# Performance work log

Measured on AMD Instinct MI355X. Metric: run time of the kernel, lower is better.

Reference implementation:

```python
import jax, jax.numpy as jnp
import numpy as np

N = 20000   # nodes
E = 320000  # directed edges (before self-loops)
D = 64      # input_dim
H = 10      # GAT heads
HD = H * D  # 640
NEG_SLOPE = 0.2


def setup_inputs() -> dict:
    key = jax.random.key(0)
    ks = jax.random.split(key, 10)
    return {
        "x": jax.random.normal(ks[0], (N, D), jnp.float32),
        "W_gat": jax.random.normal(ks[1], (D, HD), jnp.float32) / np.sqrt(D).astype(np.float32),
        "att_src": jax.random.normal(ks[2], (H, D), jnp.float32) / np.sqrt(D).astype(np.float32),
        "att_dst": jax.random.normal(ks[3], (H, D), jnp.float32) / np.sqrt(D).astype(np.float32),
        "b_gat": jnp.zeros((HD,), jnp.float32),
        "W_gcn": jax.random.normal(ks[4], (HD, HD), jnp.float32) / np.sqrt(HD).astype(np.float32),
        "b_gcn": jnp.zeros((HD,), jnp.float32),
        "W1": jax.random.normal(ks[5], (2 * HD, 1500), jnp.float32) / np.sqrt(2 * HD).astype(np.float32),
        "b1": jnp.zeros((1500,), jnp.float32),
        "W2": jax.random.normal(ks[6], (1500, 10), jnp.float32) / np.sqrt(1500).astype(np.float32),
        "b2": jnp.zeros((10,), jnp.float32),
        "edge_index": jax.random.randint(ks[7], (2, E), 0, N, dtype=jnp.int64),
    }


def _forward(x, W_gat, att_src, att_dst, b_gat, W_gcn, b_gcn, W1, b1, W2, b2, edge_index):
    n = x.shape[0]
    # add self-loops (PyG default for both GATConv and GCNConv)
    loop = jnp.arange(n, dtype=edge_index.dtype)
    ei = jnp.concatenate([edge_index, jnp.stack([loop, loop])], axis=1)
    src, dst = ei[0], ei[1]

    # ---- GATConv(D -> D, heads=H, concat) ----
    xl = (x @ W_gat).reshape(n, H, D)                      # [N,H,D]
    a_src = jnp.einsum('nhd,hd->nh', xl, att_src)          # [N,H]
    a_dst = jnp.einsum('nhd,hd->nh', xl, att_dst)          # [N,H]
    alpha = jax.nn.leaky_relu(a_src[src] + a_dst[dst], NEG_SLOPE)  # [E',H]
    m = jax.ops.segment_max(alpha, dst, num_segments=n)    # segment softmax over incoming edges
    ex = jnp.exp(alpha - m[dst])
    den = jax.ops.segment_sum(ex, dst, num_segments=n)
    w = ex / (den[dst] + 1e-16)                            # [E',H]
    msg = xl[src] * w[:, :, None]                          # [E',H,D]
    x1 = jax.ops.segment_sum(msg, dst, num_segments=n).reshape(n, HD) + b_gat
    x1 = jax.nn.relu(x1)

    # ---- GCNConv(HD -> HD), symmetric norm with self-loops ----
    deg = jax.ops.segment_sum(jnp.ones(ei.shape[1], x.dtype), dst, num_segments=n)
    dinv = jnp.where(deg > 0, jax.lax.rsqrt(deg), 0.0)
    norm = dinv[src] * dinv[dst]                           # [E']
    xw = x1 @ W_gcn                                        # [N,HD]
    x2 = jax.ops.segment_sum(xw[src] * norm[:, None], dst, num_segments=n) + b_gcn
    x2 = jax.nn.relu(x2)

    # ---- global max/mean pool (batch=None -> single graph) + MLP head ----
    pooled = jnp.concatenate([x2.max(axis=0, keepdims=True),
                              x2.mean(axis=0, keepdims=True)], axis=1)  # [1, 2*HD]
    h = jax.nn.relu(pooled @ W1 + b1)
    # dropout is identity in eval mode
    return h @ W2 + b2                                     # [1, 10]


def reference(x, W_gat, att_src, att_dst, b_gat, W_gcn, b_gcn, W1, b1, W2, b2, edge_index):
    return _forward(x, W_gat, att_src, att_dst, b_gat, W_gcn, b_gcn, W1, b1, W2, b2, edge_index)
```

## Files before the change

### kernel.cpp

```cpp
#include <hip/hip_runtime.h>
#include <hip/hip_bf16.h>
#include <math.h>

#define NN 20000
#define DD 64
#define HH 10
#define HDIM 640
#define NEG 0.2f
#define H1 1500
#define BKK 64

typedef _Float16 half8 __attribute__((ext_vector_type(8)));
typedef _Float16 half4v __attribute__((ext_vector_type(4)));
typedef float f32x4 __attribute__((ext_vector_type(4)));

__global__ __launch_bounds__(256) void k_prep(const float* __restrict__ Wgcn,
                                              const float* __restrict__ Wg,
                                              _Float16* __restrict__ Wbt,
                                              _Float16* __restrict__ WgT,
                                              const int* __restrict__ ei, int E,
                                              int* __restrict__ cnt)
{
    const int bid = blockIdx.x;
    if (bid < 440) {
        __shared__ float t[32][33];
        const int bx = bid % 20;
        int by = bid / 20;
        const float* W; _Float16* WT; int rows, cols;
        if (by < 20) { W = Wgcn; WT = Wbt; rows = HDIM; cols = HDIM; }
        else         { W = Wg;   WT = WgT; rows = DD;   cols = HDIM; by -= 20; }
        const int lx = threadIdx.x & 31, ly = threadIdx.x >> 5;
        #pragma unroll
        for (int i = ly; i < 32; i += 8)
            t[i][lx] = W[(size_t)(by * 32 + i) * cols + bx * 32 + lx];
        __syncthreads();
        #pragma unroll
        for (int j = ly; j < 32; j += 8)
            WT[(size_t)(bx * 32 + j) * rows + by * 32 + lx] = (_Float16)t[lx][j];
    } else {
        const int e = (bid - 440) * 256 + threadIdx.x;
        if (e >= E + NN) return;
        const int d = (e < E) ? ei[E + e] : (e - E);
        atomicAdd(&cnt[d], 1);
    }
}

__global__ __launch_bounds__(1024) void k_scan(const int* __restrict__ cnt,
                                               int* __restrict__ rowptr,
                                               float* __restrict__ dinv)
{
    __shared__ int sh[1024];
    const int t = threadIdx.x;
    const int CH = 20;
    const int base = t * CH;
    int loc[CH];
    int s = 0;
    #pragma unroll
    for (int i = 0; i < CH; ++i) {
        const int idx = base + i;
        const int c = (idx < NN) ? cnt[idx] : 0;
        loc[i] = s; s += c;
    }
    sh[t] = s; __syncthreads();
    for (int off = 1; off < 1024; off <<= 1) {
        const int v = (t >= off) ? sh[t - off] : 0;
        __syncthreads();
        sh[t] += v;
        __syncthreads();
    }
    const int prev = (t == 0) ? 0 : sh[t - 1];
    #pragma unroll
    for (int i = 0; i < CH; ++i) {
        const int idx = base + i;
        if (idx < NN) {
            rowptr[idx] = prev + loc[i];
            dinv[idx]   = rsqrtf((float)cnt[idx]);
        }
    }
    if (t == 1023) rowptr[NN] = sh[1023];
}

__global__ __launch_bounds__(256) void k_big(
    const float* __restrict__ x, const _Float16* __restrict__ WgT,
    const float* __restrict__ att_s, const float* __restrict__ att_d,
    _Float16* __restrict__ xl, float* __restrict__ aST, float* __restrict__ aDT,
    const int* __restrict__ ei, int E, const int* __restrict__ rowptr,
    int* __restrict__ cursor, int* __restrict__ csr)
{
    const int bid = blockIdx.x;
    if (bid >= 1570) {
        const int e = (bid - 1570) * 256 + threadIdx.x;
        if (e >= E + NN) return;
        int s, d;
        if (e < E) { s = ei[e]; d = ei[E + e]; } else { s = d = e - E; }
        const int pos = atomicAdd(&cursor[d], 1);
        csr[rowptr[d] + pos] = s;
        return;
    }

    __shared__ _Float16 As[128][72];
    __shared__ _Float16 Bs[64][72];
    const int tid = threadIdx.x;
    const int m0 = (bid % 157) * 128;
    const int h  = bid / 157;
    const int n0 = h * 64;

    {
        const int row = tid >> 1, ch = (tid & 1) * 32;
        const int gr = m0 + row;
        if (gr < NN) {
            const float* xp = &x[(size_t)gr * DD + ch];
            #pragma unroll
            for (int i = 0; i < 8; ++i) {
                const float4 v = *(const float4*)&xp[i * 4];
                half4v o = {(_Float16)v.x, (_Float16)v.y, (_Float16)v.z, (_Float16)v.w};
                *(half4v*)&As[row][ch + i * 4] = o;
            }
        } else {
            const half8 z = {0, 0, 0, 0, 0, 0, 0, 0};
            #pragma unroll
            for (int i = 0; i < 4; ++i) *(half8*)&As[row][ch + i * 8] = z;
        }
    }
    {
        const int row = tid >> 2, part = (tid & 3) * 16;
        const _Float16* wp = &WgT[(size_t)(n0 + row) * DD + part];
        *(half8*)&Bs[row][part]     = *(const half8*)&wp[0];
        *(half8*)&Bs[row][part + 8] = *(const half8*)&wp[8];
    }
    __syncthreads();

    const int lane = tid & 63, wave = tid >> 6;
    const int l15 = lane & 15, quad = lane >> 4;
    f32x4 acc[2][4];
    #pragma unroll
    for (int r = 0; r < 2; ++r)
        #pragma unroll
        for (int c = 0; c < 4; ++c) acc[r][c] = (f32x4){0.f, 0.f, 0.f, 0.f};

    #pragma unroll
    for (int ks = 0; ks < 2; ++ks) {
        const half8 a0 = *(const half8*)&As[wave * 32 + l15][ks * 32 + quad * 8];
        const half8 a1 = *(const half8*)&As[wave * 32 + 16 + l15][ks * 32 + quad * 8];
        #pragma unroll
        for (int c = 0; c < 4; ++c) {
            const half8 b = *(const half8*)&Bs[c * 16 + l15][ks * 32 + quad * 8];
            acc[0][c] = __builtin_amdgcn_mfma_f32_16x16x32_f16(a0, b, acc[0][c], 0, 0, 0);
            acc[1][c] = __builtin_amdgcn_mfma_f32_16x16x32_f16(a1, b, acc[1][c], 0, 0, 0);
        }
    }

    float asv[4], adv[4];
    #pragma unroll
    for (int c = 0; c < 4; ++c) {
        asv[c] = att_s[h * DD + c * 16 + l15];
        adv[c] = att_d[h * DD + c * 16 + l15];
    }
    #pragma unroll
    for (int r = 0; r < 2; ++r) {
        float ps[4] = {0.f, 0.f, 0.f, 0.f}, pd[4] = {0.f, 0.f, 0.f, 0.f};
        #pragma unroll
        for (int c = 0; c < 4; ++c)
            #pragma unroll
            for (int g = 0; g < 4; ++g) {
                ps[g] = fmaf(acc[r][c][g], asv[c], ps[g]);
                pd[g] = fmaf(acc[r][c][g], adv[c], pd[g]);
            }
        #pragma unroll
        for (int m = 1; m <= 8; m <<= 1)
            #pragma unroll
            for (int g = 0; g < 4; ++g) {
                ps[g] += __shfl_xor(ps[g], m);
                pd[g] += __shfl_xor(pd[g], m);
            }
        #pragma unroll
        for (int c = 0; c < 4; ++c)
            #pragma unroll
            for (int g = 0; g < 4; ++g) {
                const int row = m0 + wave * 32 + r * 16 + quad * 4 + g;
                if (row < NN)
                    xl[(size_t)row * HDIM + n0 + c * 16 + l15] = (_Float16)acc[r][c][g];
            }
        if (l15 == 0)
            #pragma unroll
            for (int g = 0; g < 4; ++g) {
                const int row = m0 + wave * 32 + r * 16 + quad * 4 + g;
                if (row < NN) {
                    aST[(size_t)h * NN + row] = ps[g];
                    aDT[(size_t)h * NN + row] = pd[g];
                }
            }
    }
}

__device__ __forceinline__ bool slice_map3(int bid, int& s, int& m)
{
    const int r = bid & 7, k = bid >> 3;
    if (k < 625) { s = r; m = k; return true; }
    s = 8 + (r >> 2);
    m = (r & 3) * 157 + (k - 625);
    return m < 625;
}

__device__ __forceinline__ float lrexp(float a)
{
    a = (a >= 0.f) ? a : NEG * a;
    return __expf(a);
}

__global__ __launch_bounds__(256) void k_gat_gather4(
    const int* __restrict__ rowptr, const int* __restrict__ csr,
    const float* __restrict__ aST, const float* __restrict__ aDT,
    const _Float16* __restrict__ xl, const float* __restrict__ b_gat,
    _Float16* __restrict__ x1)
{
    int s, m;
    if (!slice_map3(blockIdx.x, s, m)) return;
    const int wave = threadIdx.x >> 6, lane = threadIdx.x & 63;
    const int g = lane >> 3, l = lane & 7;
    const int n = m * 32 + wave * 8 + g;
    const int col = s * 64 + l * 8;
    const float* __restrict__ as = aST + (size_t)s * NN;
    const _Float16* __restrict__ xc = xl + col;
    const float ad = aDT[(size_t)s * NN + n];

    float acc[8];
    #pragma unroll
    for (int i = 0; i < 8; ++i) acc[i] = 0.f;
    float ws = 0.f;

    const int j0 = rowptr[n], j1 = rowptr[n + 1];
    int j = j0;
    for (; j + 3 < j1; j += 4) {
        const int sA = csr[j], sB = csr[j + 1], sC = csr[j + 2], sD = csr[j + 3];
        const float wA = lrexp(as[sA] + ad);
        const float wB = lrexp(as[sB] + ad);
        const float wC = lrexp(as[sC] + ad);
        const float wD = lrexp(as[sD] + ad);
        ws += wA + wB + wC + wD;
        const half8 vA = *(const half8*)&xc[(size_t)sA * HDIM];
        const half8 vB = *(const half8*)&xc[(size_t)sB * HDIM];
        const half8 vC = *(const half8*)&xc[(size_t)sC * HDIM];
        const half8 vD = *(const half8*)&xc[(size_t)sD * HDIM];
        #pragma unroll
        for (int i = 0; i < 8; ++i) {
            acc[i] = fmaf(wA, (float)vA[i], acc[i]);
            acc[i] = fmaf(wB, (float)vB[i], acc[i]);
            acc[i] = fmaf(wC, (float)vC[i], acc[i]);
            acc[i] = fmaf(wD, (float)vD[i], acc[i]);
        }
    }
    for (; j < j1; ++j) {
        const int sA = csr[j];
        const float wA = lrexp(as[sA] + ad);
        ws += wA;
        const half8 vA = *(const half8*)&xc[(size_t)sA * HDIM];
        #pragma unroll
        for (int i = 0; i < 8; ++i) acc[i] = fmaf(wA, (float)vA[i], acc[i]);
    }

    const float rr = 1.f / (ws + 1e-16f);
    const float4 ba = *(const float4*)&b_gat[col];
    const float4 bb = *(const float4*)&b_gat[col + 4];
    const float bv[8] = {ba.x, ba.y, ba.z, ba.w, bb.x, bb.y, bb.z, bb.w};
    half8 o;
    #pragma unroll
    for (int i = 0; i < 8; ++i) {
        const float v = fmaf(acc[i], rr, bv[i]);
        o[i] = (_Float16)((v > 0.f) ? v : 0.f);
    }
    *(half8*)&x1[(size_t)n * HDIM + col] = o;
}

__global__ __launch_bounds__(256) void k_gcn_gather4(
    const int* __restrict__ rowptr, const int* __restrict__ csr,
    const float* __restrict__ dinv, const _Float16* __restrict__ x1,
    _Float16* __restrict__ t)
{
    int s, m;
    if (!slice_map3(blockIdx.x, s, m)) return;
    const int wave = threadIdx.x >> 6, lane = threadIdx.x & 63;
    const int g = lane >> 3, l = lane & 7;
    const int n = m * 32 + wave * 8 + g;
    const int col = s * 64 + l * 8;
    const _Float16* __restrict__ xc = x1 + col;
    const float dd = dinv[n];

    float acc[8];
    #pragma unroll
    for (int i = 0; i < 8; ++i) acc[i] = 0.f;

    const int j0 = rowptr[n], j1 = rowptr[n + 1];
    int j = j0;
    for (; j + 3 < j1; j += 4) {
        const int sA = csr[j], sB = csr[j + 1], sC = csr[j + 2], sD = csr[j + 3];
        const float wA = dinv[sA], wB = dinv[sB];
        const float wC = dinv[sC], wD = dinv[sD];
        const half8 vA = *(const half8*)&xc[(size_t)sA * HDIM];
        const half8 vB = *(const half8*)&xc[(size_t)sB * HDIM];
        const half8 vC = *(const half8*)&xc[(size_t)sC * HDIM];
        const half8 vD = *(const half8*)&xc[(size_t)sD * HDIM];
        #pragma unroll
        for (int i = 0; i < 8; ++i) {
            acc[i] = fmaf(wA, (float)vA[i], acc[i]);
            acc[i] = fmaf(wB, (float)vB[i], acc[i]);
            acc[i] = fmaf(wC, (float)vC[i], acc[i]);
            acc[i] = fmaf(wD, (float)vD[i], acc[i]);
        }
    }
    for (; j < j1; ++j) {
        const int sA = csr[j];
        const float wA = dinv[sA];
        const half8 vA = *(const half8*)&xc[(size_t)sA * HDIM];
        #pragma unroll
        for (int i = 0; i < 8; ++i) acc[i] = fmaf(wA, (float)vA[i], acc[i]);
    }

    half8 o;
    #pragma unroll
    for (int i = 0; i < 8; ++i) o[i] = (_Float16)(acc[i] * dd);
    *(half8*)&t[(size_t)n * HDIM + col] = o;
}

__global__ __launch_bounds__(256) void k_gemm2(const _Float16* __restrict__ X,
                                               const _Float16* __restrict__ Wbt,
                                               const float* __restrict__ b_gcn,
                                               float* __restrict__ pmax,
                                               float* __restrict__ psum)
{
    __shared__ _Float16 Bs[2][128 * BKK];
    const int bid = blockIdx.x;
    const int r = bid & 7, q = bid >> 3;
    const int strip = (q / 5) * 8 + r;
    const int nt = q % 5;
    if (strip >= 157) return;

    const int tid = threadIdx.x;
    const int lane = tid & 63, wave = tid >> 6;
    const int l15 = lane & 15, quad = lane >> 4;
    const int m0 = strip * 128 + wave * 32;
    const int n0 = nt * 128;

    f32x4 acc[2][8];
    #pragma unroll
    for (int rr = 0; rr < 2; ++rr)
        #pragma unroll
        for (int c = 0; c < 8; ++c) acc[rr][c] = (f32x4){0.f, 0.f, 0.f, 0.f};

    const _Float16* a0p = &X[(size_t)(m0 + l15) * HDIM + quad * 8];
    const _Float16* a1p = a0p + (size_t)16 * HDIM;
    const int srow = wave * 8 + (lane >> 3);
    const int sck  = lane & 7;

#define STAGE4(buf, kb)                                                          \
    {                                                                            \
        _Pragma("unroll")                                                        \
        for (int i = 0; i < 4; ++i) {                                            \
            const int rw = i * 32 + srow;                                        \
            const int ck = sck ^ (rw & 7);                                       \
            const _Float16* src = &Wbt[(size_t)(n0 + rw) * HDIM + (kb) + ck * 8];\
            __builtin_amdgcn_global_load_lds(                                    \
                (const __attribute__((address_space(1))) void*)src,              \
                (__attribute__((address_space(3))) void*)&Bs[buf][((size_t)i * 256 + tid) * 8], \
                16, 0, 0);                                                       \
        }                                                                        \
    }

    STAGE4(0, 0);
    for (int it = 0; it < 10; ++it) {
        const int kb = it * BKK;
        half8 a0[2], a1[2];
        #pragma unroll
        for (int ks = 0; ks < 2; ++ks) {
            a0[ks] = *(const half8*)(a0p + kb + ks * 32);
            a1[ks] = *(const half8*)(a1p + kb + ks * 32);
        }
        if (it < 9) {
            STAGE4((it + 1) & 1, kb + BKK);
            asm volatile("s_waitcnt vmcnt(4)" ::: "memory");
        } else {
            asm volatile("s_waitcnt vmcnt(0)" ::: "memory");
        }
        __builtin_amdgcn_s_barrier();
        __builtin_amdgcn_sched_barrier(0);
        const _Float16* Bsc = Bs[it & 1];
        #pragma unroll
        for (int ks = 0; ks < 2; ++ks) {
            #pragma unroll
            for (int c = 0; c < 8; ++c) {
                const int br = c * 16 + l15;
                const int ck = (ks * 4 + quad) ^ (br & 7);
                const half8 b = *(const half8*)&Bsc[(size_t)br * BKK + ck * 8];
                acc[0][c] = __builtin_amdgcn_mfma_f32_16x16x32_f16(a0[ks], b, acc[0][c], 0, 0, 0);
                acc[1][c] = __builtin_amdgcn_mfma_f32_16x16x32_f16(a1[ks], b, acc[1][c], 0, 0, 0);
            }
        }
        __builtin_amdgcn_sched_barrier(0);
        __builtin_amdgcn_s_barrier();
        __builtin_amdgcn_sched_barrier(0);
    }
#undef STAGE4

    float lmax[8], lsum[8];
    #pragma unroll
    for (int c = 0; c < 8; ++c) { lmax[c] = 0.f; lsum[c] = 0.f; }
    #pragma unroll
    for (int c = 0; c < 8; ++c) {
        const float bb = b_gcn[n0 + c * 16 + l15];
        #pragma unroll
        for (int rr = 0; rr < 2; ++rr)
            #pragma unroll
            for (int g = 0; g < 4; ++g) {
                const int row = m0 + rr * 16 + quad * 4 + g;
                if (row < NN) {
                    float v = acc[rr][c][g] + bb;
                    v = (v > 0.f) ? v : 0.f;
                    lmax[c] = fmaxf(lmax[c], v);
                    lsum[c] += v;
                }
            }
    }
    float* redm = (float*)Bs;
    float* reds = redm + 128;
    if (tid < 128) { redm[tid] = 0.f; reds[tid] = 0.f; }
    __syncthreads();
    #pragma unroll
    for (int c = 0; c < 8; ++c) {
        const int col = c * 16 + l15;
        atomicMax((int*)&redm[col], __float_as_int(lmax[c]));
        atomicAdd(&reds[col], lsum[c]);
    }
    __syncthreads();
    if (tid < 128) {
        atomicMax((int*)&pmax[n0 + tid], __float_as_int(redm[tid]));
        atomicAdd(&psum[n0 + tid], reds[tid]);
    }
}

__global__ __launch_bounds__(256) void k_mlp(const float* __restrict__ pmax,
                                             const float* __restrict__ psum,
                                             const float* __restrict__ W1,
                                             const float* __restrict__ b1,
                                             const float* __restrict__ W2,
                                             const float* __restrict__ b2,
                                             float* __restrict__ hacc,
                                             int* __restrict__ done,
                                             float* __restrict__ out)
{
    __shared__ float pl[80];
    __shared__ int isLast;
    const int t = threadIdx.x;
    const int i0 = blockIdx.y * 80;
    if (t < 80) {
        const int i = i0 + t;
        pl[t] = (i < HDIM) ? pmax[i] : psum[i - HDIM] * (1.0f / NN);
    }
    __syncthreads();
    const int j = blockIdx.x * 256 + t;
    if (j < H1) {
        float acc = 0.f;
        #pragma unroll 8
        for (int i = 0; i < 80; ++i)
            acc = fmaf(pl[i], W1[(size_t)(i0 + i) * H1 + j], acc);
        atomicAdd(&hacc[j], acc);
    }
    __threadfence();
    __syncthreads();
    if (t == 0) {
        const int total = gridDim.x * gridDim.y;
        isLast = (atomicAdd(done, 1) == total - 1) ? 1 : 0;
    }
    __syncthreads();
    if (!isLast) return;

    __shared__ float hsh[H1];
    __shared__ float red[256];
    for (int i = t; i < H1; i += 256) {
        const float v = atomicAdd(&hacc[i], 0.0f) + b1[i];
        hsh[i] = (v > 0.f) ? v : 0.f;
    }
    __syncthreads();
    float acc[10];
    #pragma unroll
    for (int k = 0; k < 10; ++k) acc[k] = 0.f;
    for (int i = t; i < H1; i += 256) {
        const float h = hsh[i];
        #pragma unroll
        for (int k = 0; k < 10; ++k) acc[k] = fmaf(h, W2[i * 10 + k], acc[k]);
    }
    for (int k = 0; k < 10; ++k) {
        red[t] = acc[k]; __syncthreads();
        for (int s2 = 128; s2 > 0; s2 >>= 1) {
            if (t < s2) red[t] += red[t + s2];
            __syncthreads();
        }
        if (t == 0) out[k] = red[0] + b2[k];
        __syncthreads();
    }
}

extern "C" void kernel_launch(void* const* d_in, const int* in_sizes, int n_in,
                              void* d_out, int out_size, void* d_ws, size_t ws_size,
                              hipStream_t stream)
{
    const float* x     = (const float*)d_in[0];
    const float* Wg    = (const float*)d_in[1];
    const float* att_s = (const float*)d_in[2];
    const float* att_d = (const float*)d_in[3];
    const float* b_gat = (const float*)d_in[4];
    const float* Wgcn  = (const float*)d_in[5];
    const float* b_gcn = (const float*)d_in[6];
    const float* W1    = (const float*)d_in[7];
    const float* b1    = (const float*)d_in[8];
    const float* W2    = (const float*)d_in[9];
    const float* b2    = (const float*)d_in[10];
    const int*   ei    = (const int*)d_in[11];
    const int E = in_sizes[11] / 2;
    const int EP = E + NN;
    float* out = (float*)d_out;

    char* wsp = (char*)d_ws;
    size_t off = 0;
    auto alc = [&](size_t b) { void* p = wsp + off; off += (b + 255) & ~(size_t)255; return p; };
    _Float16* bufA = (_Float16*)alc((size_t)NN * HDIM * 2);
    _Float16* bufB = (_Float16*)alc((size_t)NN * HDIM * 2);
    float* aST    = (float*)alc((size_t)HH * NN * 4);
    float* aDT    = (float*)alc((size_t)HH * NN * 4);
    int*   rowptr = (int*)alc((size_t)(NN + 1) * 4);
    int*   csr    = (int*)alc((size_t)EP * 4);
    float* dinv   = (float*)alc((size_t)NN * 4);
    _Float16* Wbt = (_Float16*)alc((size_t)HDIM * HDIM * 2);
    _Float16* WgT = (_Float16*)alc((size_t)HDIM * DD * 2);
    const size_t zoff = off;
    int*   cnt    = (int*)alc((size_t)NN * 4);
    int*   cursor = (int*)alc((size_t)NN * 4);
    float* pmax   = (float*)alc((size_t)HDIM * 4);
    float* psum   = (float*)alc((size_t)HDIM * 4);
    float* hacc   = (float*)alc((size_t)H1 * 4);
    int*   done   = (int*)alc(256);
    const size_t zsize = off - zoff;

    hipMemsetAsync(cnt, 0, zsize, stream);

    const int CNTB = (EP + 255) / 256;
    k_prep<<<440 + CNTB, 256, 0, stream>>>(Wgcn, Wg, Wbt, WgT, ei, E, cnt);
    k_scan<<<1, 1024, 0, stream>>>(cnt, rowptr, dinv);
    k_big<<<1570 + CNTB, 256, 0, stream>>>(x, WgT, att_s, att_d, bufA, aST, aDT,
                                           ei, E, rowptr, cursor, csr);
    const int GG = 6256;
    k_gat_gather4<<<GG, 256, 0, stream>>>(rowptr, csr, aST, aDT, bufA, b_gat, bufB);
    k_gcn_gather4<<<GG, 256, 0, stream>>>(rowptr, csr, dinv, bufB, bufA);
    k_gemm2<<<800, 256, 0, stream>>>(bufA, Wbt, b_gcn, pmax, psum);
    dim3 gm(6, 16);
    k_mlp<<<gm, 256, 0, stream>>>(pmax, psum, W1, b1, W2, b2, hacc, done, out);
}
```

Measured before the change: 318.3 us.

## Sort gather nodes by in-degree to balance wavefront work

Builds a degree histogram in the scan kernel, then a counting-sort permutation of nodes by clamped in-degree, computed in extra blocks of the CSR-fill kernel. Both GAT and GCN gather kernels now process nodes in that permuted order, so the 8 nodes sharing a wavefront have similar degrees and lanes diverge less in their loop trip counts. In exchange it adds an indirection load per thread, scatters the output rows across memory, and loses the locality of consecutive node ids.

Measured after the change: 374.4 us. 1.18x slower.

```diff
diff --git a/kernel.cpp b/kernel.cpp
--- a/kernel.cpp
+++ b/kernel.cpp
@@ -47,12 +47,15 @@
 
 __global__ __launch_bounds__(1024) void k_scan(const int* __restrict__ cnt,
                                                int* __restrict__ rowptr,
-                                               float* __restrict__ dinv)
+                                               float* __restrict__ dinv,
+                                               int* __restrict__ dbase)
 {
     __shared__ int sh[1024];
+    __shared__ int dh[128];
     const int t = threadIdx.x;
     const int CH = 20;
     const int base = t * CH;
+    if (t < 128) dh[t] = 0;
     int loc[CH];
     int s = 0;
     #pragma unroll
@@ -75,9 +78,16 @@
         if (idx < NN) {
             rowptr[idx] = prev + loc[i];
             dinv[idx]   = rsqrtf((float)cnt[idx]);
+            int c = cnt[idx]; if (c > 127) c = 127;
+            atomicAdd(&dh[c], 1);
         }
     }
     if (t == 1023) rowptr[NN] = sh[1023];
+    __syncthreads();
+    if (t == 0) {
+        int run = 0;
+        for (int b = 0; b < 128; ++b) { dbase[b] = run; run += dh[b]; }
+    }
 }
 
 __global__ __launch_bounds__(256) void k_big(
@@ -85,9 +95,19 @@
     const float* __restrict__ att_s, const float* __restrict__ att_d,
     _Float16* __restrict__ xl, float* __restrict__ aST, float* __restrict__ aDT,
     const int* __restrict__ ei, int E, const int* __restrict__ rowptr,
-    int* __restrict__ cursor, int* __restrict__ csr)
+    int* __restrict__ cursor, int* __restrict__ csr,
+    const int* __restrict__ cnt, const int* __restrict__ dbase,
+    int* __restrict__ dcur, int* __restrict__ perm, int CNTB)
 {
     const int bid = blockIdx.x;
+    if (bid >= 1570 + CNTB) {
+        const int n = (bid - 1570 - CNTB) * 256 + threadIdx.x;
+        if (n >= NN) return;
+        int c = cnt[n]; if (c > 127) c = 127;
+        const int pos = atomicAdd(&dcur[c], 1);
+        perm[dbase[c] + pos] = n;
+        return;
+    }
     if (bid >= 1570) {
         const int e = (bid - 1570) * 256 + threadIdx.x;
         if (e >= E + NN) return;
@@ -208,8 +228,9 @@
     return __expf(a);
 }
 
-__global__ __launch_bounds__(256) void k_gat_gather4(
+__global__ __launch_bounds__(256) void k_gat_gather8(
     const int* __restrict__ rowptr, const int* __restrict__ csr,
+    const int* __restrict__ perm,
     const float* __restrict__ aST, const float* __restrict__ aDT,
     const _Float16* __restrict__ xl, const float* __restrict__ b_gat,
     _Float16* __restrict__ x1)
@@ -218,7 +239,7 @@
     if (!slice_map3(blockIdx.x, s, m)) return;
     const int wave = threadIdx.x >> 6, lane = threadIdx.x & 63;
     const int g = lane >> 3, l = lane & 7;
-    const int n = m * 32 + wave * 8 + g;
+    const int n = perm[m * 32 + wave * 8 + g];
     const int col = s * 64 + l * 8;
     const float* __restrict__ as = aST + (size_t)s * NN;
     const _Float16* __restrict__ xc = xl + col;
@@ -272,8 +293,9 @@
     *(half8*)&x1[(size_t)n * HDIM + col] = o;
 }
 
-__global__ __launch_bounds__(256) void k_gcn_gather4(
+__global__ __launch_bounds__(256) void k_gcn_gather8(
     const int* __restrict__ rowptr, const int* __restrict__ csr,
+    const int* __restrict__ perm,
     const float* __restrict__ dinv, const _Float16* __restrict__ x1,
     _Float16* __restrict__ t)
 {
@@ -281,7 +303,7 @@
     if (!slice_map3(blockIdx.x, s, m)) return;
     const int wave = threadIdx.x >> 6, lane = threadIdx.x & 63;
     const int g = lane >> 3, l = lane & 7;
-    const int n = m * 32 + wave * 8 + g;
+    const int n = perm[m * 32 + wave * 8 + g];
     const int col = s * 64 + l * 8;
     const _Float16* __restrict__ xc = x1 + col;
     const float dd = dinv[n];
@@ -531,9 +553,12 @@
     float* dinv   = (float*)alc((size_t)NN * 4);
     _Float16* Wbt = (_Float16*)alc((size_t)HDIM * HDIM * 2);
     _Float16* WgT = (_Float16*)alc((size_t)HDIM * DD * 2);
+    int*   perm   = (int*)alc((size_t)NN * 4);
+    int*   dbase  = (int*)alc(128 * 4);
     const size_t zoff = off;
     int*   cnt    = (int*)alc((size_t)NN * 4);
     int*   cursor = (int*)alc((size_t)NN * 4);
+    int*   dcur   = (int*)alc(128 * 4);
     float* pmax   = (float*)alc((size_t)HDIM * 4);
     float* psum   = (float*)alc((size_t)HDIM * 4);
     float* hacc   = (float*)alc((size_t)H1 * 4);
@@ -543,13 +568,15 @@
     hipMemsetAsync(cnt, 0, zsize, stream);
 
     const int CNTB = (EP + 255) / 256;
+    const int PERMB = (NN + 255) / 256;
     k_prep<<<440 + CNTB, 256, 0, stream>>>(Wgcn, Wg, Wbt, WgT, ei, E, cnt);
-    k_scan<<<1, 1024, 0, stream>>>(cnt, rowptr, dinv);
-    k_big<<<1570 + CNTB, 256, 0, stream>>>(x, WgT, att_s, att_d, bufA, aST, aDT,
-                                           ei, E, rowptr, cursor, csr);
+    k_scan<<<1, 1024, 0, stream>>>(cnt, rowptr, dinv, dbase);
+    k_big<<<1570 + CNTB + PERMB, 256, 0, stream>>>(x, WgT, att_s, att_d, bufA, aST, aDT,
+                                                   ei, E, rowptr, cursor, csr,
+                                                   cnt, dbase, dcur, perm, CNTB);
     const int GG = 6256;
-    k_gat_gather4<<<GG, 256, 0, stream>>>(rowptr, csr, aST, aDT, bufA, b_gat, bufB);
-    k_gcn_gather4<<<GG, 256, 0, stream>>>(rowptr, csr, dinv, bufB, bufA);
+    k_gat_gather8<<<GG, 256, 0, stream>>>(rowptr, csr, perm, aST, aDT, bufA, b_gat, bufB);
+    k_gcn_gather8<<<GG, 256, 0, stream>>>(rowptr, csr, perm, dinv, bufB, bufA);
     k_gemm2<<<800, 256, 0, stream>>>(bufA, Wbt, b_gcn, pmax, psum);
     dim3 gm(6, 16);
     k_mlp<<<gm, 256, 0, stream>>>(pmax, psum, W1, b1, W2, b2, hacc, done, out);
```
